# Optimization experiments

Measured on AMD Instinct MI355X. Metric: run time of the kernel, lower is better.

Reference implementation:

```python
import jax, jax.numpy as jnp
import numpy as np

N, E, D, K, H = 100000, 1600000, 32, 3, 1


def setup_inputs() -> dict:
    key = jax.random.key(0)
    ks = jax.random.split(key, 7)
    return {
        "src": jax.random.randint(ks[0], (E,), 0, N),
        "dst": jax.random.randint(ks[1], (E,), 0, N),
        "embedding": jax.random.normal(ks[2], (N, D), jnp.float32),
        "lambda_max": jnp.full((1,), 2.0, jnp.float32),
        # ChebConv: single Linear(k*d -> d) over concatenated Chebyshev terms (shared by both calls)
        "cheb_W": jax.random.normal(ks[3], (K * D, D), jnp.float32) / np.sqrt(K * D),
        "cheb_b": jnp.zeros((D,), jnp.float32),
        # GATv2: fc_src / fc_dst Linear(d -> H*d) + attention vector (H, d)
        "gat_W_src": jax.random.normal(ks[4], (D, H * D), jnp.float32) / np.sqrt(D),
        "gat_b_src": jnp.zeros((H * D,), jnp.float32),
        "gat_W_dst": jax.random.normal(ks[5], (D, H * D), jnp.float32) / np.sqrt(D),
        "gat_b_dst": jnp.zeros((H * D,), jnp.float32),
        "gat_attn": jax.random.normal(ks[6], (H, D), jnp.float32) / np.sqrt(D),
    }


def _cheb(src, dst, feat, lam, W, b, n):
    # DGL ChebConv with lambda_max given; activation = leaky_relu (slope 0.01)
    deg = jnp.clip(jax.ops.segment_sum(jnp.ones(src.shape[0], feat.dtype), dst, num_segments=n), 1.0)
    dinv = deg[:, None] ** -0.5  # D^{-1/2}, (N,1)
    re_norm = 2.0 / lam[0]

    def unnL(f):  # D^{-1/2} A D^{-1/2} f
        return jax.ops.segment_sum((f * dinv)[src], dst, num_segments=n) * dinv

    X0 = feat
    X1 = -re_norm * unnL(X0) + X0 * (re_norm - 1.0)
    Xs = [X0, X1]
    for _ in range(2, K):
        Xi = -2.0 * re_norm * unnL(X1) + X1 * (2.0 * (re_norm - 1.0)) - X0
        Xs.append(Xi)
        X0, X1 = X1, Xi
    return jax.nn.leaky_relu(jnp.concatenate(Xs, axis=1) @ W + b, 0.01)


def _gatv2(src, dst, h, Ws, bs, Wd, bd, attn, n):
    Hh, Dd = attn.shape
    fs = (h @ Ws + bs).reshape(n, Hh, Dd)  # feat_src 'el'
    fd = (h @ Wd + bd).reshape(n, Hh, Dd)  # feat_dst 'er'
    e = jax.nn.leaky_relu(fs[src] + fd[dst], 0.2)        # (E,H,D), GATv2 negative_slope=0.2
    logits = jnp.einsum('ehd,hd->eh', e, attn)           # (E,H)
    m = jax.ops.segment_max(logits, dst, num_segments=n)  # per-dst softmax (edge_softmax)
    ex = jnp.exp(logits - m[dst])
    a = ex / jax.ops.segment_sum(ex, dst, num_segments=n)[dst]
    ft = jax.ops.segment_sum(fs[src] * a[..., None], dst, num_segments=n)  # (N,H,D)
    return jax.nn.leaky_relu(ft, 0.01)  # activation=F.leaky_relu


def reference(src, dst, embedding, lambda_max, cheb_W, cheb_b,
              gat_W_src, gat_b_src, gat_W_dst, gat_b_dst, gat_attn):
    n, d = embedding.shape
    h = _cheb(src, dst, embedding, lambda_max, cheb_W, cheb_b, n)
    h = _cheb(src, dst, h, lambda_max, cheb_W, cheb_b, n)
    out = _gatv2(src, dst, h, gat_W_src, gat_b_src, gat_W_dst, gat_b_dst, gat_attn, n)
    return out.reshape(-1, d)
```

## Files before the change

### kernel.cpp

```cpp
#include <hip/hip_runtime.h>

#define TPB 256
#define NB 512
#define CAPB 4096
#define CHUNK 4096
#define CAPS 5120

__global__ void k_zero_u(unsigned int* p, int n){
  int i = blockIdx.x*TPB + threadIdx.x;
  if(i < n) p[i] = 0u;
}

__global__ void k_scan1(const unsigned int* deg, unsigned int* ptr,
                        unsigned int* bsum, int N){
  __shared__ unsigned int s[TPB];
  int i = blockIdx.x*TPB + threadIdx.x;
  unsigned int v = (i < N) ? deg[i] : 0u;
  s[threadIdx.x] = v; __syncthreads();
  for(int off = 1; off < TPB; off <<= 1){
    unsigned int x = (threadIdx.x >= off) ? s[threadIdx.x - off] : 0u;
    __syncthreads();
    s[threadIdx.x] += x;
    __syncthreads();
  }
  if(i < N) ptr[i] = s[threadIdx.x] - v;
  if(threadIdx.x == TPB-1) bsum[blockIdx.x] = s[TPB-1];
}

__global__ void k_scan2(unsigned int* bsum, int nb){
  __shared__ unsigned int s[TPB];
  __shared__ unsigned int carry;
  if(threadIdx.x == 0) carry = 0u;
  __syncthreads();
  for(int base = 0; base < nb; base += TPB){
    int i = base + threadIdx.x;
    unsigned int v = (i < nb) ? bsum[i] : 0u;
    s[threadIdx.x] = v; __syncthreads();
    for(int off = 1; off < TPB; off <<= 1){
      unsigned int x = (threadIdx.x >= off) ? s[threadIdx.x - off] : 0u;
      __syncthreads();
      s[threadIdx.x] += x;
      __syncthreads();
    }
    if(i < nb) bsum[i] = s[threadIdx.x] - v + carry;
    __syncthreads();
    if(threadIdx.x == 0) carry += s[TPB-1];
    __syncthreads();
  }
}

__global__ void k_scan3(unsigned int* ptr, const unsigned int* bsum, int N, int E){
  int i = blockIdx.x*TPB + threadIdx.x;
  if(i < N) ptr[i] += bsum[blockIdx.x];
  if(i == 0) ptr[N] = (unsigned int)E;
}

__global__ __launch_bounds__(TPB) void k_bin1(const int* src, const int* dst,
    unsigned int* btail, int2* binned, int E, int npb){
  __shared__ unsigned int hist[NB];
  __shared__ unsigned int base[NB];
  int t = threadIdx.x;
  for(int i = t; i < NB; i += TPB) hist[i] = 0u;
  __syncthreads();
  int e0 = blockIdx.x*CHUNK;
  int e1 = e0 + CHUNK; if(e1 > E) e1 = E;
  for(int e = e0 + t; e < e1; e += TPB)
    atomicAdd(&hist[dst[e]/npb], 1u);
  __syncthreads();
  for(int i = t; i < NB; i += TPB){
    unsigned int c = hist[i];
    base[i] = c ? atomicAdd(btail + i, c) : 0u;
    hist[i] = 0u;
  }
  __syncthreads();
  for(int e = e0 + t; e < e1; e += TPB){
    int d = dst[e];
    int b = d / npb;
    unsigned int off = base[b] + atomicAdd(&hist[b], 1u);
    if(off < CAPB) binned[(size_t)b*CAPB + off] = make_int2(src[e], d);
  }
}

__global__ __launch_bounds__(TPB) void k_cnt(const int2* binned, const unsigned int* btail,
    unsigned int* deg, float* dinv, int npb, int N){
  __shared__ unsigned int c[TPB];
  int b = blockIdx.x;
  int n0 = b*npb;
  int t = threadIdx.x;
  c[t] = 0u;
  __syncthreads();
  unsigned int cnt = btail[b]; if(cnt > (unsigned)CAPB) cnt = CAPB;
  const int2* eb = binned + (size_t)b*CAPB;
  for(unsigned int i = t; i < cnt; i += TPB)
    atomicAdd(&c[eb[i].y - n0], 1u);
  __syncthreads();
  int n = n0 + t;
  if(t < npb && n < N){
    unsigned int d = c[t];
    deg[n] = d;
    dinv[n] = 1.0f / sqrtf(fmaxf((float)d, 1.0f));
  }
}

__global__ __launch_bounds__(TPB) void k_bin2(const int2* binned,
    const unsigned int* ptr, int* csr, int npb, int N){
  __shared__ unsigned int curs[256];
  __shared__ int stage[CAPS];
  int b = blockIdx.x;
  int n0 = b*npb; if(n0 >= N) return;
  int n1 = n0 + npb; if(n1 > N) n1 = N;
  int t = threadIdx.x;
  unsigned int segbase = ptr[n0];
  unsigned int seglen  = ptr[n1] - segbase;
  for(int i = n0 + t; i < n1; i += TPB) curs[i - n0] = ptr[i] - segbase;
  __syncthreads();
  unsigned int cnt = seglen < (unsigned)CAPB ? seglen : (unsigned)CAPB;
  const int2* eb = binned + (size_t)b*CAPB;
  if(seglen <= (unsigned)CAPS){
    for(unsigned int i = t; i < cnt; i += TPB){
      int2 sd = eb[i];
      unsigned int p0 = atomicAdd(&curs[sd.y - n0], 1u);
      stage[p0] = sd.x;
    }
    __syncthreads();
    for(unsigned int i = t; i < seglen; i += TPB) csr[segbase + i] = stage[i];
  } else {
    for(unsigned int i = t; i < cnt; i += TPB){
      int2 sd = eb[i];
      unsigned int p0 = atomicAdd(&curs[sd.y - n0], 1u);
      csr[segbase + p0] = sd.x;
    }
  }
}

__device__ __forceinline__ float4 agg_gather4(const unsigned int* ptr, const int* csr,
    const float* X, const float* dinv, int t, int lane){
  int g  = lane >> 3;
  int f4 = (lane & 7) << 2;
  unsigned int p0 = ptr[t], p1 = ptr[t+1];
  float4 S0 = make_float4(0.f,0.f,0.f,0.f);
  float4 S1 = make_float4(0.f,0.f,0.f,0.f);
  for(unsigned int base = p0; base < p1; base += 32){
    int idx = 0; float dva = 0.f;
    unsigned int pos = base + (unsigned)lane;
    if(pos < p1){ idx = csr[pos]; dva = dinv[idx]; }
    unsigned int cnt = p1 - base; if(cnt > 32u) cnt = 32u;
    unsigned int rounds = (cnt + 3u) >> 2;
    for(unsigned int r = 0; r < rounds; r += 2){
      int el0 = (int)(r << 2) + g;
      int s0  = __shfl(idx, el0, 32);
      float d0 = __shfl(dva, el0, 32);
      const float4 x0 = *(const float4*)(X + (size_t)s0*32 + f4);
      if(r + 1 < rounds){
        int el1 = el0 + 4;
        int s1  = __shfl(idx, el1, 32);
        float d1 = __shfl(dva, el1, 32);
        const float4 x1 = *(const float4*)(X + (size_t)s1*32 + f4);
        S1.x += x1.x*d1; S1.y += x1.y*d1; S1.z += x1.z*d1; S1.w += x1.w*d1;
      }
      S0.x += x0.x*d0; S0.y += x0.y*d0; S0.z += x0.z*d0; S0.w += x0.w*d0;
    }
  }
  float4 S;
  S.x = S0.x + S1.x; S.y = S0.y + S1.y; S.z = S0.z + S1.z; S.w = S0.w + S1.w;
  S.x += __shfl_xor(S.x, 8, 32);  S.y += __shfl_xor(S.y, 8, 32);
  S.z += __shfl_xor(S.z, 8, 32);  S.w += __shfl_xor(S.w, 8, 32);
  S.x += __shfl_xor(S.x, 16, 32); S.y += __shfl_xor(S.y, 16, 32);
  S.z += __shfl_xor(S.z, 16, 32); S.w += __shfl_xor(S.w, 16, 32);
  return S;
}

__global__ __launch_bounds__(TPB) void k_cheb1(const unsigned int* ptr, const int* csr,
    const float* X0, const float* dinv, const float* lam, float* X1, int N){
  int t = blockIdx.x*8 + (threadIdx.x >> 5);
  if(t >= N) return;
  int lane = threadIdx.x & 31;
  float4 S = agg_gather4(ptr, csr, X0, dinv, t, lane);
  if((lane >> 3) != 0) return;
  int f4 = (lane & 7) << 2;
  float re = 2.0f / lam[0];
  float dt = dinv[t];
  size_t o = (size_t)t*32 + f4;
  const float4 x0 = *(const float4*)(X0 + o);
  float4 r;
  r.x = -re*(S.x*dt) + (re-1.0f)*x0.x;
  r.y = -re*(S.y*dt) + (re-1.0f)*x0.y;
  r.z = -re*(S.z*dt) + (re-1.0f)*x0.z;
  r.w = -re*(S.w*dt) + (re-1.0f)*x0.w;
  *(float4*)(X1 + o) = r;
}

__global__ __launch_bounds__(TPB) void k_cheb2(const unsigned int* ptr, const int* csr,
    const float* X0, const float* X1, const float* dinv, const float* lam,
    float* X2, int N){
  int t = blockIdx.x*8 + (threadIdx.x >> 5);
  if(t >= N) return;
  int lane = threadIdx.x & 31;
  float4 S = agg_gather4(ptr, csr, X1, dinv, t, lane);
  if((lane >> 3) != 0) return;
  int f4 = (lane & 7) << 2;
  float re = 2.0f / lam[0];
  float dt = dinv[t];
  size_t o = (size_t)t*32 + f4;
  const float4 x0 = *(const float4*)(X0 + o);
  const float4 x1 = *(const float4*)(X1 + o);
  float c1 = -2.0f*re, c2 = 2.0f*(re-1.0f);
  float4 r;
  r.x = c1*(S.x*dt) + c2*x1.x - x0.x;
  r.y = c1*(S.y*dt) + c2*x1.y - x0.y;
  r.z = c1*(S.z*dt) + c2*x1.z - x0.z;
  r.w = c1*(S.w*dt) + c2*x1.w - x0.w;
  *(float4*)(X2 + o) = r;
}

__global__ __launch_bounds__(TPB) void k_lin(const float* X0, const float* X1,
    const float* X2, const float* W, const float* b, float* out, int N){
  int n = blockIdx.x*TPB + threadIdx.x;
  if(n >= N) return;
  float acc[32];
  #pragma unroll
  for(int c = 0; c < 32; c++) acc[c] = b[c];
  const float* xs0 = X0 + (size_t)n*32;
  const float* xs1 = X1 + (size_t)n*32;
  const float* xs2 = X2 + (size_t)n*32;
  #pragma unroll
  for(int s3 = 0; s3 < 3; s3++){
    const float4* xp = (const float4*)(s3 == 0 ? xs0 : (s3 == 1 ? xs1 : xs2));
    #pragma unroll
    for(int q = 0; q < 8; q++){
      float4 xv = xp[q];
      const float* Wr = W + (size_t)(s3*32 + q*4)*32;
      #pragma unroll
      for(int c = 0; c < 32; c++)
        acc[c] += xv.x*Wr[c] + xv.y*Wr[32+c] + xv.z*Wr[64+c] + xv.w*Wr[96+c];
    }
  }
  float4* op = (float4*)(out + (size_t)n*32);
  #pragma unroll
  for(int q = 0; q < 8; q++){
    float4 v;
    float a;
    a = acc[4*q+0]; v.x = a > 0.f ? a : 0.01f*a;
    a = acc[4*q+1]; v.y = a > 0.f ? a : 0.01f*a;
    a = acc[4*q+2]; v.z = a > 0.f ? a : 0.01f*a;
    a = acc[4*q+3]; v.w = a > 0.f ? a : 0.01f*a;
    op[q] = v;
  }
}

__global__ __launch_bounds__(TPB) void k_fc(const float* h,
    const float* Wsr, const float* bsr, const float* Wds, const float* bds,
    float* fs, float* fd, int N){
  int n = blockIdx.x*TPB + threadIdx.x;
  if(n >= N) return;
  float as[32], ad[32];
  #pragma unroll
  for(int c = 0; c < 32; c++){ as[c] = bsr[c]; ad[c] = bds[c]; }
  const float4* xp = (const float4*)(h + (size_t)n*32);
  #pragma unroll
  for(int q = 0; q < 8; q++){
    float4 xv = xp[q];
    const float* Wr = Wsr + (size_t)(q*4)*32;
    const float* Vr = Wds + (size_t)(q*4)*32;
    #pragma unroll
    for(int c = 0; c < 32; c++){
      as[c] += xv.x*Wr[c] + xv.y*Wr[32+c] + xv.z*Wr[64+c] + xv.w*Wr[96+c];
      ad[c] += xv.x*Vr[c] + xv.y*Vr[32+c] + xv.z*Vr[64+c] + xv.w*Vr[96+c];
    }
  }
  float4* sp = (float4*)(fs + (size_t)n*32);
  float4* dp = (float4*)(fd + (size_t)n*32);
  #pragma unroll
  for(int q = 0; q < 8; q++){
    float4 v1, v2;
    v1.x = as[4*q+0]; v1.y = as[4*q+1]; v1.z = as[4*q+2]; v1.w = as[4*q+3];
    v2.x = ad[4*q+0]; v2.y = ad[4*q+1]; v2.z = ad[4*q+2]; v2.w = ad[4*q+3];
    sp[q] = v1;
    dp[q] = v2;
  }
}

__global__ __launch_bounds__(TPB) void k_gat(const unsigned int* ptr, const int* csr,
    const float* fs, const float* fd, const float* attn, float* out, int N){
  int t = blockIdx.x*8 + (threadIdx.x >> 5);
  if(t >= N) return;
  int lane = threadIdx.x & 31;
  int g  = lane >> 3;
  int f4 = (lane & 7) << 2;
  unsigned int p0 = ptr[t], p1 = ptr[t+1];
  const float4 fd4 = *(const float4*)(fd + (size_t)t*32 + f4);
  const float4 at4 = *(const float4*)(attn + f4);
  float m = -3.402823466e38f, den = 0.f;
  float4 acc = make_float4(0.f,0.f,0.f,0.f);
  for(unsigned int base = p0; base < p1; base += 32){
    int idx = 0;
    unsigned int pos = base + (unsigned)lane;
    if(pos < p1) idx = csr[pos];
    unsigned int cnt = p1 - base; if(cnt > 32u) cnt = 32u;
    unsigned int rounds = (cnt + 3u) >> 2;
    for(unsigned int r = 0; r < rounds; r++){
      int el = (int)(r << 2) + g;
      int s  = __shfl(idx, el, 32);
      const float4 f = *(const float4*)(fs + (size_t)s*32 + f4);
      float vx = f.x + fd4.x; vx = vx > 0.f ? vx : 0.2f*vx;
      float vy = f.y + fd4.y; vy = vy > 0.f ? vy : 0.2f*vy;
      float vz = f.z + fd4.z; vz = vz > 0.f ? vz : 0.2f*vz;
      float vw = f.w + fd4.w; vw = vw > 0.f ? vw : 0.2f*vw;
      float pl = vx*at4.x + vy*at4.y + vz*at4.z + vw*at4.w;
      pl += __shfl_xor(pl, 4, 32);
      pl += __shfl_xor(pl, 2, 32);
      pl += __shfl_xor(pl, 1, 32);
      if(el < (int)cnt){
        float mn = fmaxf(m, pl);
        float sc = __expf(m - mn);
        float e  = __expf(pl - mn);
        den = den*sc + e;
        acc.x = acc.x*sc + f.x*e;
        acc.y = acc.y*sc + f.y*e;
        acc.z = acc.z*sc + f.z*e;
        acc.w = acc.w*sc + f.w*e;
        m = mn;
      }
    }
  }
  #pragma unroll
  for(int off = 8; off <= 16; off <<= 1){
    float mo = __shfl_xor(m, off, 32);
    float do_ = __shfl_xor(den, off, 32);
    float ax = __shfl_xor(acc.x, off, 32);
    float ay = __shfl_xor(acc.y, off, 32);
    float az = __shfl_xor(acc.z, off, 32);
    float aw = __shfl_xor(acc.w, off, 32);
    float mn = fmaxf(m, mo);
    float a = __expf(m - mn), b = __expf(mo - mn);
    den = den*a + do_*b;
    acc.x = acc.x*a + ax*b;
    acc.y = acc.y*a + ay*b;
    acc.z = acc.z*a + az*b;
    acc.w = acc.w*a + aw*b;
    m = mn;
  }
  if(g != 0) return;
  float4 o = make_float4(0.f,0.f,0.f,0.f);
  if(den > 0.f){
    float inv = 1.0f / den;
    o.x = acc.x*inv; o.x = o.x > 0.f ? o.x : 0.01f*o.x;
    o.y = acc.y*inv; o.y = o.y > 0.f ? o.y : 0.01f*o.y;
    o.z = acc.z*inv; o.z = o.z > 0.f ? o.z : 0.01f*o.z;
    o.w = acc.w*inv; o.w = o.w > 0.f ? o.w : 0.01f*o.w;
  }
  *(float4*)(out + (size_t)t*32 + f4) = o;
}

extern "C" void kernel_launch(void* const* d_in, const int* in_sizes, int n_in,
                              void* d_out, int out_size, void* d_ws, size_t ws_size,
                              hipStream_t stream){
  const int*   src = (const int*)d_in[0];
  const int*   dst = (const int*)d_in[1];
  const float* emb = (const float*)d_in[2];
  const float* lam = (const float*)d_in[3];
  const float* cW  = (const float*)d_in[4];
  const float* cB  = (const float*)d_in[5];
  const float* gWs = (const float*)d_in[6];
  const float* gbs = (const float*)d_in[7];
  const float* gWd = (const float*)d_in[8];
  const float* gbd = (const float*)d_in[9];
  const float* gat = (const float*)d_in[10];
  const int E  = in_sizes[0];
  const int N  = in_sizes[2] / 32;
  const int NF = N * 32;
  const int npb = (N + NB - 1) / NB;

  int gN  = (N + TPB-1)/TPB;
  int gR  = (N + 7)/8;
  int gB1 = (E + CHUNK-1)/CHUNK;

  char* p = (char*)d_ws;
  auto alloc = [&](size_t bytes)->char*{ char* r = p; p += (bytes + 255) & ~(size_t)255; return r; };
  unsigned int* degi = (unsigned int*)alloc((size_t)N*4);
  unsigned int* ptrA = (unsigned int*)alloc((size_t)(N+1)*4);
  unsigned int* btail= (unsigned int*)alloc((size_t)NB*4);
  unsigned int* bsum = (unsigned int*)alloc((size_t)(gN+1)*4);
  float* dinv = (float*)alloc((size_t)N*4);
  int*   csr  = (int*)alloc((size_t)E*4);
  float* X1   = (float*)alloc((size_t)NF*4);
  float* X2   = (float*)alloc((size_t)NF*4);
  float* h1   = (float*)alloc((size_t)NF*4);
  float* h2   = (float*)alloc((size_t)NF*4);
  int2* binned = (int2*)X1;

  k_zero_u<<<(NB+TPB-1)/TPB, TPB, 0, stream>>>(btail, NB);
  k_bin1<<<gB1, TPB, 0, stream>>>(src, dst, btail, binned, E, npb);
  k_cnt<<<NB, TPB, 0, stream>>>(binned, btail, degi, dinv, npb, N);
  k_scan1<<<gN, TPB, 0, stream>>>(degi, ptrA, bsum, N);
  k_scan2<<<1,  TPB, 0, stream>>>(bsum, gN);
  k_scan3<<<gN, TPB, 0, stream>>>(ptrA, bsum, N, E);
  k_bin2<<<NB,  TPB, 0, stream>>>(binned, ptrA, csr, npb, N);

  k_cheb1<<<gR, TPB, 0, stream>>>(ptrA, csr, emb, dinv, lam, X1, N);
  k_cheb2<<<gR, TPB, 0, stream>>>(ptrA, csr, emb, X1, dinv, lam, X2, N);
  k_lin<<<gN, TPB, 0, stream>>>(emb, X1, X2, cW, cB, h1, N);

  k_cheb1<<<gR, TPB, 0, stream>>>(ptrA, csr, h1, dinv, lam, X1, N);
  k_cheb2<<<gR, TPB, 0, stream>>>(ptrA, csr, h1, X1, dinv, lam, X2, N);
  k_lin<<<gN, TPB, 0, stream>>>(h1, X1, X2, cW, cB, h2, N);

  k_fc<<<gN, TPB, 0, stream>>>(h2, gWs, gbs, gWd, gbd, X1 , X2 , N);
  k_gat<<<gR, TPB, 0, stream>>>(ptrA, csr, X1, X2, gat, (float*)d_out, N);
}
```

Baseline: 377.5 us.

## Replace binned CSR build with atomic counting sort and fuse second linear into GAT fc

Replaces the two-pass bucketed binning CSR construction with a global-atomic degree count, a scan that also computes dinv and resets counters, and an atomic scatter into CSR. It also fuses the second Chebyshev linear layer with the GATv2 source/destination projections, so the intermediate h2 is never written to or read from memory. The atomic scatter produces an unordered neighbor order within each row and relies on global atomics with heavy contention and random writes, where the old version staged writes in shared memory. The fused kernel keeps more live registers per thread.

Measured after the change: 564.6 us. +49.6%, slower.

```diff
diff --git a/kernel.cpp b/kernel.cpp
--- a/kernel.cpp
+++ b/kernel.cpp
@@ -1,18 +1,19 @@
 #include <hip/hip_runtime.h>
 
 #define TPB 256
-#define NB 512
-#define CAPB 4096
-#define CHUNK 4096
-#define CAPS 5120
 
 __global__ void k_zero_u(unsigned int* p, int n){
   int i = blockIdx.x*TPB + threadIdx.x;
   if(i < n) p[i] = 0u;
 }
 
-__global__ void k_scan1(const unsigned int* deg, unsigned int* ptr,
-                        unsigned int* bsum, int N){
+__global__ __launch_bounds__(TPB) void k_deg(const int* dst, unsigned int* deg, int E){
+  int e = blockIdx.x*TPB + threadIdx.x;
+  if(e < E) atomicAdd(&deg[dst[e]], 1u);
+}
+
+__global__ void k_scan1(unsigned int* deg, unsigned int* ptr,
+                        unsigned int* bsum, float* dinv, int N){
   __shared__ unsigned int s[TPB];
   int i = blockIdx.x*TPB + threadIdx.x;
   unsigned int v = (i < N) ? deg[i] : 0u;
@@ -23,7 +24,11 @@
     s[threadIdx.x] += x;
     __syncthreads();
   }
-  if(i < N) ptr[i] = s[threadIdx.x] - v;
+  if(i < N){
+    ptr[i] = s[threadIdx.x] - v;
+    dinv[i] = 1.0f / sqrtf(fmaxf((float)v, 1.0f));
+    deg[i] = 0u;
+  }
   if(threadIdx.x == TPB-1) bsum[blockIdx.x] = s[TPB-1];
 }
 
@@ -55,82 +60,13 @@
   if(i == 0) ptr[N] = (unsigned int)E;
 }
 
-__global__ __launch_bounds__(TPB) void k_bin1(const int* src, const int* dst,
-    unsigned int* btail, int2* binned, int E, int npb){
-  __shared__ unsigned int hist[NB];
-  __shared__ unsigned int base[NB];
-  int t = threadIdx.x;
-  for(int i = t; i < NB; i += TPB) hist[i] = 0u;
-  __syncthreads();
-  int e0 = blockIdx.x*CHUNK;
-  int e1 = e0 + CHUNK; if(e1 > E) e1 = E;
-  for(int e = e0 + t; e < e1; e += TPB)
-    atomicAdd(&hist[dst[e]/npb], 1u);
-  __syncthreads();
-  for(int i = t; i < NB; i += TPB){
-    unsigned int c = hist[i];
-    base[i] = c ? atomicAdd(btail + i, c) : 0u;
-    hist[i] = 0u;
-  }
-  __syncthreads();
-  for(int e = e0 + t; e < e1; e += TPB){
-    int d = dst[e];
-    int b = d / npb;
-    unsigned int off = base[b] + atomicAdd(&hist[b], 1u);
-    if(off < CAPB) binned[(size_t)b*CAPB + off] = make_int2(src[e], d);
-  }
-}
-
-__global__ __launch_bounds__(TPB) void k_cnt(const int2* binned, const unsigned int* btail,
-    unsigned int* deg, float* dinv, int npb, int N){
-  __shared__ unsigned int c[TPB];
-  int b = blockIdx.x;
-  int n0 = b*npb;
-  int t = threadIdx.x;
-  c[t] = 0u;
-  __syncthreads();
-  unsigned int cnt = btail[b]; if(cnt > (unsigned)CAPB) cnt = CAPB;
-  const int2* eb = binned + (size_t)b*CAPB;
-  for(unsigned int i = t; i < cnt; i += TPB)
-    atomicAdd(&c[eb[i].y - n0], 1u);
-  __syncthreads();
-  int n = n0 + t;
-  if(t < npb && n < N){
-    unsigned int d = c[t];
-    deg[n] = d;
-    dinv[n] = 1.0f / sqrtf(fmaxf((float)d, 1.0f));
-  }
-}
-
-__global__ __launch_bounds__(TPB) void k_bin2(const int2* binned,
-    const unsigned int* ptr, int* csr, int npb, int N){
-  __shared__ unsigned int curs[256];
-  __shared__ int stage[CAPS];
-  int b = blockIdx.x;
-  int n0 = b*npb; if(n0 >= N) return;
-  int n1 = n0 + npb; if(n1 > N) n1 = N;
-  int t = threadIdx.x;
-  unsigned int segbase = ptr[n0];
-  unsigned int seglen  = ptr[n1] - segbase;
-  for(int i = n0 + t; i < n1; i += TPB) curs[i - n0] = ptr[i] - segbase;
-  __syncthreads();
-  unsigned int cnt = seglen < (unsigned)CAPB ? seglen : (unsigned)CAPB;
-  const int2* eb = binned + (size_t)b*CAPB;
-  if(seglen <= (unsigned)CAPS){
-    for(unsigned int i = t; i < cnt; i += TPB){
-      int2 sd = eb[i];
-      unsigned int p0 = atomicAdd(&curs[sd.y - n0], 1u);
-      stage[p0] = sd.x;
-    }
-    __syncthreads();
-    for(unsigned int i = t; i < seglen; i += TPB) csr[segbase + i] = stage[i];
-  } else {
-    for(unsigned int i = t; i < cnt; i += TPB){
-      int2 sd = eb[i];
-      unsigned int p0 = atomicAdd(&curs[sd.y - n0], 1u);
-      csr[segbase + p0] = sd.x;
-    }
-  }
+__global__ __launch_bounds__(TPB) void k_scatter(const int* src, const int* dst,
+    const unsigned int* ptr, unsigned int* cur, int* csr, int E){
+  int e = blockIdx.x*TPB + threadIdx.x;
+  if(e >= E) return;
+  int d = dst[e];
+  unsigned int o = atomicAdd(&cur[d], 1u);
+  csr[ptr[d] + o] = src[e];
 }
 
 __device__ __forceinline__ float4 agg_gather4(const unsigned int* ptr, const int* csr,
@@ -248,24 +184,47 @@
   }
 }
 
-__global__ __launch_bounds__(TPB) void k_fc(const float* h,
+__global__ __launch_bounds__(TPB) void k_lin_fc(const float* X0, const float* X1,
+    const float* X2, const float* W, const float* b,
     const float* Wsr, const float* bsr, const float* Wds, const float* bds,
     float* fs, float* fd, int N){
   int n = blockIdx.x*TPB + threadIdx.x;
   if(n >= N) return;
+  float acc[32];
+  #pragma unroll
+  for(int c = 0; c < 32; c++) acc[c] = b[c];
+  const float* xs0 = X0 + (size_t)n*32;
+  const float* xs1 = X1 + (size_t)n*32;
+  const float* xs2 = X2 + (size_t)n*32;
+  #pragma unroll
+  for(int s3 = 0; s3 < 3; s3++){
+    const float4* xp = (const float4*)(s3 == 0 ? xs0 : (s3 == 1 ? xs1 : xs2));
+    #pragma unroll
+    for(int q = 0; q < 8; q++){
+      float4 xv = xp[q];
+      const float* Wr = W + (size_t)(s3*32 + q*4)*32;
+      #pragma unroll
+      for(int c = 0; c < 32; c++)
+        acc[c] += xv.x*Wr[c] + xv.y*Wr[32+c] + xv.z*Wr[64+c] + xv.w*Wr[96+c];
+    }
+  }
+  #pragma unroll
+  for(int c = 0; c < 32; c++){
+    float a = acc[c];
+    acc[c] = a > 0.f ? a : 0.01f*a;
+  }
   float as[32], ad[32];
   #pragma unroll
   for(int c = 0; c < 32; c++){ as[c] = bsr[c]; ad[c] = bds[c]; }
-  const float4* xp = (const float4*)(h + (size_t)n*32);
   #pragma unroll
   for(int q = 0; q < 8; q++){
-    float4 xv = xp[q];
+    float hx = acc[4*q+0], hy = acc[4*q+1], hz = acc[4*q+2], hw = acc[4*q+3];
     const float* Wr = Wsr + (size_t)(q*4)*32;
     const float* Vr = Wds + (size_t)(q*4)*32;
     #pragma unroll
     for(int c = 0; c < 32; c++){
-      as[c] += xv.x*Wr[c] + xv.y*Wr[32+c] + xv.z*Wr[64+c] + xv.w*Wr[96+c];
-      ad[c] += xv.x*Vr[c] + xv.y*Vr[32+c] + xv.z*Vr[64+c] + xv.w*Vr[96+c];
+      as[c] += hx*Wr[c] + hy*Wr[32+c] + hz*Wr[64+c] + hw*Wr[96+c];
+      ad[c] += hx*Vr[c] + hy*Vr[32+c] + hz*Vr[64+c] + hw*Vr[96+c];
     }
   }
   float4* sp = (float4*)(fs + (size_t)n*32);
@@ -369,33 +328,30 @@
   const int E  = in_sizes[0];
   const int N  = in_sizes[2] / 32;
   const int NF = N * 32;
-  const int npb = (N + NB - 1) / NB;
 
   int gN  = (N + TPB-1)/TPB;
   int gR  = (N + 7)/8;
-  int gB1 = (E + CHUNK-1)/CHUNK;
+  int gE  = (E + TPB-1)/TPB;
 
   char* p = (char*)d_ws;
   auto alloc = [&](size_t bytes)->char*{ char* r = p; p += (bytes + 255) & ~(size_t)255; return r; };
   unsigned int* degi = (unsigned int*)alloc((size_t)N*4);
   unsigned int* ptrA = (unsigned int*)alloc((size_t)(N+1)*4);
-  unsigned int* btail= (unsigned int*)alloc((size_t)NB*4);
   unsigned int* bsum = (unsigned int*)alloc((size_t)(gN+1)*4);
   float* dinv = (float*)alloc((size_t)N*4);
   int*   csr  = (int*)alloc((size_t)E*4);
   float* X1   = (float*)alloc((size_t)NF*4);
   float* X2   = (float*)alloc((size_t)NF*4);
   float* h1   = (float*)alloc((size_t)NF*4);
-  float* h2   = (float*)alloc((size_t)NF*4);
-  int2* binned = (int2*)X1;
-
-  k_zero_u<<<(NB+TPB-1)/TPB, TPB, 0, stream>>>(btail, NB);
-  k_bin1<<<gB1, TPB, 0, stream>>>(src, dst, btail, binned, E, npb);
-  k_cnt<<<NB, TPB, 0, stream>>>(binned, btail, degi, dinv, npb, N);
-  k_scan1<<<gN, TPB, 0, stream>>>(degi, ptrA, bsum, N);
+  float* fs   = (float*)alloc((size_t)NF*4);
+  float* fd   = (float*)alloc((size_t)NF*4);
+
+  k_zero_u<<<gN, TPB, 0, stream>>>(degi, N);
+  k_deg<<<gE, TPB, 0, stream>>>(dst, degi, E);
+  k_scan1<<<gN, TPB, 0, stream>>>(degi, ptrA, bsum, dinv, N);
   k_scan2<<<1,  TPB, 0, stream>>>(bsum, gN);
   k_scan3<<<gN, TPB, 0, stream>>>(ptrA, bsum, N, E);
-  k_bin2<<<NB,  TPB, 0, stream>>>(binned, ptrA, csr, npb, N);
+  k_scatter<<<gE, TPB, 0, stream>>>(src, dst, ptrA, degi, csr, E);
 
   k_cheb1<<<gR, TPB, 0, stream>>>(ptrA, csr, emb, dinv, lam, X1, N);
   k_cheb2<<<gR, TPB, 0, stream>>>(ptrA, csr, emb, X1, dinv, lam, X2, N);
@@ -403,8 +359,7 @@
 
   k_cheb1<<<gR, TPB, 0, stream>>>(ptrA, csr, h1, dinv, lam, X1, N);
   k_cheb2<<<gR, TPB, 0, stream>>>(ptrA, csr, h1, X1, dinv, lam, X2, N);
-  k_lin<<<gN, TPB, 0, stream>>>(h1, X1, X2, cW, cB, h2, N);
-
-  k_fc<<<gN, TPB, 0, stream>>>(h2, gWs, gbs, gWd, gbd, X1 , X2 , N);
-  k_gat<<<gR, TPB, 0, stream>>>(ptrA, csr, X1, X2, gat, (float*)d_out, N);
-}
+  k_lin_fc<<<gN, TPB, 0, stream>>>(h1, X1, X2, cW, cB, gWs, gbs, gWd, gbd, fs, fd, N);
+
+  k_gat<<<gR, TPB, 0, stream>>>(ptrA, csr, fs, fd, gat, (float*)d_out, N);
+}
```
